# Kernel optimization log

Measured on AMD Instinct MI355X. Metric: run time of the kernel, lower is better.

Reference implementation:

```python
import jax, jax.numpy as jnp
import numpy as np

BATCH, N_IN, N_OUT, DEGREE = 128, 2048, 1024, 15
EPSILON = 1.0
TEMPERATURE = 0.1
NEG_FILL = -1000000000.0


def setup_inputs() -> dict:
    key = jax.random.key(0)
    k1, k2, k3 = jax.random.split(key, 3)
    x = jax.random.normal(k1, (BATCH, N_IN), dtype=jnp.float32)
    weights = jax.random.normal(k2, (N_OUT, N_IN), dtype=jnp.float32) * 0.02
    # buffer: (rand(n_out, n_in) < degree/n_in).float()
    synaptic_mask = (jax.random.uniform(k3, (N_OUT, N_IN)) < DEGREE / N_IN).astype(jnp.float32)
    return {"x": x, "weights": weights, "synaptic_mask": synaptic_mask}


def reference(x, weights, synaptic_mask):
    n_in = x.shape[1]
    # torch.median returns the LOWER of the two middle values for even n:
    # sorted index (n-1)//2
    consensus = jnp.sort(x, axis=1)[:, (n_in - 1) // 2][:, None]  # [B, 1]
    gate = (jnp.abs(x - consensus) < EPSILON).astype(x.dtype)      # [B, n_in]
    gated_x = x * gate                                             # [B, n_in]
    # dense broadcast-add: [B, n_out, n_in]
    combined = gated_x[:, None, :] + weights[None, :, :]
    masked_z = jnp.where(synaptic_mask == 0.0, NEG_FILL, combined)
    return TEMPERATURE * jax.nn.logsumexp(masked_z / TEMPERATURE, axis=2)  # [B, n_out]
```

## Files before the change

### kernel.cpp

```cpp
#include <hip/hip_runtime.h>
#include <math.h>

#define BATCH 128
#define N_IN 2048
#define N_OUT 1024
#define MAXK 40
#define BCAP 64
#define TEMP 0.1f
#define INV_TEMP 10.0f
#define NEG_FILL -1.0e9f
#define WLO -0.1875f
#define WHI 0.1875f
#define BINSCALE 682.6666666f

__device__ __forceinline__ unsigned int f2key(float f) {
    unsigned int b = __float_as_uint(f);
    return (b & 0x80000000u) ? ~b : (b | 0x80000000u);
}
__device__ __forceinline__ float key2f(unsigned int u) {
    unsigned int b = (u & 0x80000000u) ? (u & 0x7FFFFFFFu) : ~u;
    return __uint_as_float(b);
}

__global__ __launch_bounds__(256) void k_med(const float* __restrict__ x,
                                             float* __restrict__ gxT) {
    __shared__ unsigned int hist[256];
    __shared__ unsigned int wsum4[4];
    __shared__ unsigned int sel[2];
    __shared__ float sbin[BCAP];
    __shared__ int s_nb;
    __shared__ float s_med;

    const int tid = threadIdx.x;
    const int lane = tid & 63;
    const int wwid = tid >> 6;
    const int b = (int)blockIdx.x;

    const float4* xr = (const float4*)(x + (size_t)b * N_IN);
    float4 va = xr[tid], vb = xr[tid + 256];
    float vals[8] = {va.x, va.y, va.z, va.w, vb.x, vb.y, vb.z, vb.w};

    hist[tid] = 0;
    if (tid == 0) s_nb = 0;
    __syncthreads();

    int cb = 0;
#pragma unroll
    for (int j = 0; j < 8; ++j) {
        float v = vals[j];
        cb += (v < WLO) ? 1 : 0;
        if (v >= WLO && v < WHI) {
            int bin = (int)((v - WLO) * BINSCALE);
            bin = (bin > 255) ? 255 : bin;
            atomicAdd(&hist[bin], 1u);
        }
    }
    int sb = cb;
#pragma unroll
    for (int off = 1; off < 64; off <<= 1) sb += __shfl_xor(sb, off, 64);
    if (lane == 0) wsum4[wwid] = (unsigned int)sb;
    __syncthreads();
    const int c_lo = (int)(wsum4[0] + wsum4[1] + wsum4[2] + wsum4[3]);
    const int R = (N_IN - 1) / 2 - c_lo;

    unsigned int hv = hist[tid];
    unsigned int sv = hv;
#pragma unroll
    for (int off = 1; off < 64; off <<= 1) {
        unsigned int t = __shfl_up(sv, off, 64);
        if (lane >= off) sv += t;
    }
    __syncthreads();
    if (lane == 63) wsum4[wwid] = sv;
    if (tid == 0) sel[0] = 0xFFFFFFFFu;
    __syncthreads();
    unsigned int base = 0;
    for (int ww = 0; ww < wwid; ++ww) base += wsum4[ww];
    const unsigned int incl = sv + base;
    const unsigned int excl = incl - hv;
    const int n_c = (int)(wsum4[0] + wsum4[1] + wsum4[2] + wsum4[3]);
    if (R >= 0 && R < n_c && (unsigned int)R >= excl && (unsigned int)R < incl) {
        sel[0] = (unsigned int)tid;
        sel[1] = (unsigned int)R - excl;
    }
    __syncthreads();

    bool fast_ok = (R >= 0 && R < n_c && sel[0] != 0xFFFFFFFFu);
    if (fast_ok) {
        const int B = (int)sel[0];
        const int r2 = (int)sel[1];
#pragma unroll
        for (int j = 0; j < 8; ++j) {
            float v = vals[j];
            if (v >= WLO && v < WHI) {
                int bin = (int)((v - WLO) * BINSCALE);
                bin = (bin > 255) ? 255 : bin;
                if (bin == B) {
                    int p = atomicAdd(&s_nb, 1);
                    if (p < BCAP) sbin[p] = v;
                }
            }
        }
        __syncthreads();
        const int nb = s_nb;
        if (nb <= BCAP) {
            if (tid < nb) {
                float v = sbin[tid];
                int nlt = 0, neq = 0;
                for (int j = 0; j < nb; ++j) {
                    float u = sbin[j];
                    nlt += (u < v) ? 1 : 0;
                    neq += (u == v) ? 1 : 0;
                }
                if (nlt <= r2 && r2 < nlt + neq) s_med = v;
            }
        } else {
            fast_ok = false;
        }
        __syncthreads();
    }
    if (!fast_ok) {
        unsigned int prefix = 0;
        unsigned int k = (N_IN - 1) / 2;
        for (int pos = 24; pos >= 0; pos -= 8) {
            hist[tid] = 0;
            __syncthreads();
            const unsigned int hmask = (pos == 24) ? 0u : (0xFFFFFFFFu << (pos + 8));
#pragma unroll
            for (int j = 0; j < 8; ++j) {
                unsigned int u = f2key(vals[j]);
                if ((u & hmask) == (prefix & hmask))
                    atomicAdd(&hist[(u >> pos) & 0xFFu], 1u);
            }
            __syncthreads();
            unsigned int v = hist[tid];
            unsigned int s2 = v;
#pragma unroll
            for (int off = 1; off < 64; off <<= 1) {
                unsigned int t = __shfl_up(s2, off, 64);
                if (lane >= off) s2 += t;
            }
            if (lane == 63) wsum4[wwid] = s2;
            __syncthreads();
            unsigned int bs = 0;
            for (int ww = 0; ww < wwid; ++ww) bs += wsum4[ww];
            const unsigned int inc2 = s2 + bs;
            const unsigned int exc2 = inc2 - v;
            if (k >= exc2 && k < inc2) {
                sel[0] = (unsigned int)tid;
                sel[1] = k - exc2;
            }
            __syncthreads();
            prefix |= sel[0] << pos;
            k = sel[1];
            __syncthreads();
        }
        if (tid == 0) s_med = key2f(prefix);
        __syncthreads();
    }
    const float med = s_med;

#pragma unroll
    for (int j = 0; j < 8; ++j) {
        const int idx = (j < 4) ? 4 * tid + j : 1024 + 4 * tid + (j - 4);
        const float v = vals[j];
        gxT[(size_t)idx * BATCH + b] = (fabsf(v - med) < 1.0f) ? v : 0.0f;
    }
}

__global__ __launch_bounds__(256) void k_clse(const float* __restrict__ w,
                                              const float* __restrict__ msk,
                                              const float* __restrict__ gxT,
                                              float* __restrict__ out) {
    __shared__ unsigned int wsum4[4];
    __shared__ int sidx[2][MAXK];
    __shared__ float swv[2][MAXK];

    const int tid = threadIdx.x;
    const int lane = tid & 63;
    const int wwid = tid >> 6;
    const int o0 = (int)blockIdx.x * 2;

    const float4* m0 = (const float4*)(msk + (size_t)o0 * N_IN);
    const float4* m1 = (const float4*)(msk + (size_t)(o0 + 1) * N_IN);
    float4 m0a = m0[tid], m0b = m0[tid + 256];
    float4 m1a = m1[tid], m1b = m1[tid + 256];
    float mv0[8] = {m0a.x, m0a.y, m0a.z, m0a.w, m0b.x, m0b.y, m0b.z, m0b.w};
    float mv1[8] = {m1a.x, m1a.y, m1a.z, m1a.w, m1b.x, m1b.y, m1b.z, m1b.w};

    int c0 = 0, c1 = 0;
#pragma unroll
    for (int j = 0; j < 8; ++j) {
        c0 += (mv0[j] != 0.0f) ? 1 : 0;
        c1 += (mv1[j] != 0.0f) ? 1 : 0;
    }
    int packed = (c0 << 16) | c1;
    int sv = packed;
#pragma unroll
    for (int off = 1; off < 64; off <<= 1) {
        int t = __shfl_up(sv, off, 64);
        if (lane >= off) sv += t;
    }
    if (lane == 63) wsum4[wwid] = (unsigned int)sv;
    __syncthreads();
    int base = 0;
    for (int ww = 0; ww < wwid; ++ww) base += (int)wsum4[ww];
    const int excl = base + sv - packed;
    const int tot = (int)(wsum4[0] + wsum4[1] + wsum4[2] + wsum4[3]);
    const int ct0 = tot >> 16;
    const int ct1 = tot & 0xFFFF;

    int p0 = (excl >> 16) & 0xFFFF;
    int p1 = excl & 0xFFFF;
#pragma unroll
    for (int j = 0; j < 8; ++j) {
        const int idx = (j < 4) ? 4 * tid + j : 1024 + 4 * tid + (j - 4);
        if (mv0[j] != 0.0f) {
            if (p0 < MAXK) sidx[0][p0] = idx;
            ++p0;
        }
        if (mv1[j] != 0.0f) {
            if (p1 < MAXK) sidx[1][p1] = idx;
            ++p1;
        }
    }
    __syncthreads();

    const int cc0 = (ct0 < MAXK) ? ct0 : MAXK;
    const int cc1 = (ct1 < MAXK) ? ct1 : MAXK;
    if (tid < cc0) swv[0][tid] = w[(size_t)o0 * N_IN + sidx[0][tid]];
    else if (tid >= 64 && tid - 64 < cc1)
        swv[1][tid - 64] = w[(size_t)(o0 + 1) * N_IN + sidx[1][tid - 64]];
    __syncthreads();

    const int oSel = tid >> 7;
    const int o = o0 + oSel;
    const int b = tid & 127;
    const int c = oSel ? ct1 : ct0;

    float res;
    if (c == 0) {
        res = NEG_FILL;
    } else if (c <= MAXK) {
        int idx = sidx[oSel][0];
        float m = (gxT[(size_t)idx * BATCH + b] + swv[oSel][0]) * INV_TEMP;
        float s = 1.0f;
        for (int j = 1; j < c; ++j) {
            idx = sidx[oSel][j];
            float v = (gxT[(size_t)idx * BATCH + b] + swv[oSel][j]) * INV_TEMP;
            float mn = fmaxf(m, v);
            s = s * __expf(m - mn) + __expf(v - mn);
            m = mn;
        }
        res = TEMP * (m + __logf(s));
    } else {
        const float* mr = msk + (size_t)o * N_IN;
        const float* wr = w + (size_t)o * N_IN;
        float m = -INFINITY, s = 0.0f;
        for (int i = 0; i < N_IN; ++i) {
            if (mr[i] != 0.0f) {
                float v = (gxT[(size_t)i * BATCH + b] + wr[i]) * INV_TEMP;
                float mn = fmaxf(m, v);
                s = s * __expf(m - mn) + __expf(v - mn);
                m = mn;
            }
        }
        res = TEMP * (m + __logf(s));
    }
    out[(size_t)b * N_OUT + o] = res;
}

extern "C" void kernel_launch(void* const* d_in, const int* in_sizes, int n_in,
                              void* d_out, int out_size, void* d_ws, size_t ws_size,
                              hipStream_t stream) {
    const float* x = (const float*)d_in[0];
    const float* w = (const float*)d_in[1];
    const float* msk = (const float*)d_in[2];
    float* out = (float*)d_out;

    float* gxT = (float*)d_ws;

    hipLaunchKernelGGL(k_med, dim3(BATCH), dim3(256), 0, stream, x, gxT);
    hipLaunchKernelGGL(k_clse, dim3(N_OUT / 2), dim3(256), 0, stream,
                       w, msk, gxT, out);
}
```

Before: 19.14 us.

## Merge median and mask compaction into one prep kernel; batch-major LSE with shared gated x

The median blocks and the mask-compaction blocks now run side by side in a single prep launch. The compaction blocks write per-output counts and a transposed (index, weight) list to workspace, so the mask scan no longer sits on the critical path after the median. The LSE kernel now assigns each block to one batch row and half the outputs. It recomputes the gated x row into shared memory, which replaces scattered gxT global reads with LDS gathers, and reads the list entries coalesced across outputs. In exchange the list loads now go to global memory instead of shared, and x is reloaded once per output half.

```diff
diff --git a/kernel.cpp b/kernel.cpp
--- a/kernel.cpp
+++ b/kernel.cpp
@@ -22,232 +22,249 @@
     return __uint_as_float(b);
 }
 
-__global__ __launch_bounds__(256) void k_med(const float* __restrict__ x,
-                                             float* __restrict__ gxT) {
+__global__ __launch_bounds__(256) void k_prep(const float* __restrict__ x,
+                                              const float* __restrict__ w,
+                                              const float* __restrict__ msk,
+                                              int* __restrict__ cnt,
+                                              int2* __restrict__ listsT,
+                                              float* __restrict__ med) {
     __shared__ unsigned int hist[256];
     __shared__ unsigned int wsum4[4];
     __shared__ unsigned int sel[2];
     __shared__ float sbin[BCAP];
     __shared__ int s_nb;
     __shared__ float s_med;
+    __shared__ int sidx[2][MAXK];
 
     const int tid = threadIdx.x;
     const int lane = tid & 63;
     const int wwid = tid >> 6;
-    const int b = (int)blockIdx.x;
-
-    const float4* xr = (const float4*)(x + (size_t)b * N_IN);
-    float4 va = xr[tid], vb = xr[tid + 256];
-    float vals[8] = {va.x, va.y, va.z, va.w, vb.x, vb.y, vb.z, vb.w};
-
-    hist[tid] = 0;
-    if (tid == 0) s_nb = 0;
-    __syncthreads();
-
-    int cb = 0;
-#pragma unroll
-    for (int j = 0; j < 8; ++j) {
-        float v = vals[j];
-        cb += (v < WLO) ? 1 : 0;
-        if (v >= WLO && v < WHI) {
-            int bin = (int)((v - WLO) * BINSCALE);
-            bin = (bin > 255) ? 255 : bin;
-            atomicAdd(&hist[bin], 1u);
-        }
-    }
-    int sb = cb;
-#pragma unroll
-    for (int off = 1; off < 64; off <<= 1) sb += __shfl_xor(sb, off, 64);
-    if (lane == 0) wsum4[wwid] = (unsigned int)sb;
-    __syncthreads();
-    const int c_lo = (int)(wsum4[0] + wsum4[1] + wsum4[2] + wsum4[3]);
-    const int R = (N_IN - 1) / 2 - c_lo;
-
-    unsigned int hv = hist[tid];
-    unsigned int sv = hv;
-#pragma unroll
-    for (int off = 1; off < 64; off <<= 1) {
-        unsigned int t = __shfl_up(sv, off, 64);
-        if (lane >= off) sv += t;
-    }
-    __syncthreads();
-    if (lane == 63) wsum4[wwid] = sv;
-    if (tid == 0) sel[0] = 0xFFFFFFFFu;
-    __syncthreads();
-    unsigned int base = 0;
-    for (int ww = 0; ww < wwid; ++ww) base += wsum4[ww];
-    const unsigned int incl = sv + base;
-    const unsigned int excl = incl - hv;
-    const int n_c = (int)(wsum4[0] + wsum4[1] + wsum4[2] + wsum4[3]);
-    if (R >= 0 && R < n_c && (unsigned int)R >= excl && (unsigned int)R < incl) {
-        sel[0] = (unsigned int)tid;
-        sel[1] = (unsigned int)R - excl;
-    }
-    __syncthreads();
-
-    bool fast_ok = (R >= 0 && R < n_c && sel[0] != 0xFFFFFFFFu);
-    if (fast_ok) {
-        const int B = (int)sel[0];
-        const int r2 = (int)sel[1];
+    const int bid = (int)blockIdx.x;
+
+    if (bid < BATCH) {
+        const int b = bid;
+        const float4* xr = (const float4*)(x + (size_t)b * N_IN);
+        float4 va = xr[tid], vb = xr[tid + 256];
+        float vals[8] = {va.x, va.y, va.z, va.w, vb.x, vb.y, vb.z, vb.w};
+
+        hist[tid] = 0;
+        if (tid == 0) s_nb = 0;
+        __syncthreads();
+
+        int cb = 0;
 #pragma unroll
         for (int j = 0; j < 8; ++j) {
             float v = vals[j];
+            cb += (v < WLO) ? 1 : 0;
             if (v >= WLO && v < WHI) {
                 int bin = (int)((v - WLO) * BINSCALE);
                 bin = (bin > 255) ? 255 : bin;
-                if (bin == B) {
-                    int p = atomicAdd(&s_nb, 1);
-                    if (p < BCAP) sbin[p] = v;
-                }
-            }
-        }
-        __syncthreads();
-        const int nb = s_nb;
-        if (nb <= BCAP) {
-            if (tid < nb) {
-                float v = sbin[tid];
-                int nlt = 0, neq = 0;
-                for (int j = 0; j < nb; ++j) {
-                    float u = sbin[j];
-                    nlt += (u < v) ? 1 : 0;
-                    neq += (u == v) ? 1 : 0;
-                }
-                if (nlt <= r2 && r2 < nlt + neq) s_med = v;
-            }
-        } else {
-            fast_ok = false;
-        }
-        __syncthreads();
+                atomicAdd(&hist[bin], 1u);
+            }
+        }
+        int sb = cb;
+#pragma unroll
+        for (int off = 1; off < 64; off <<= 1) sb += __shfl_xor(sb, off, 64);
+        if (lane == 0) wsum4[wwid] = (unsigned int)sb;
+        __syncthreads();
+        const int c_lo = (int)(wsum4[0] + wsum4[1] + wsum4[2] + wsum4[3]);
+        const int R = (N_IN - 1) / 2 - c_lo;
+
+        unsigned int hv = hist[tid];
+        unsigned int sv = hv;
+#pragma unroll
+        for (int off = 1; off < 64; off <<= 1) {
+            unsigned int t = __shfl_up(sv, off, 64);
+            if (lane >= off) sv += t;
+        }
+        __syncthreads();
+        if (lane == 63) wsum4[wwid] = sv;
+        if (tid == 0) sel[0] = 0xFFFFFFFFu;
+        __syncthreads();
+        unsigned int base = 0;
+        for (int ww = 0; ww < wwid; ++ww) base += wsum4[ww];
+        const unsigned int incl = sv + base;
+        const unsigned int excl = incl - hv;
+        const int n_c = (int)(wsum4[0] + wsum4[1] + wsum4[2] + wsum4[3]);
+        if (R >= 0 && R < n_c && (unsigned int)R >= excl && (unsigned int)R < incl) {
+            sel[0] = (unsigned int)tid;
+            sel[1] = (unsigned int)R - excl;
+        }
+        __syncthreads();
+
+        bool fast_ok = (R >= 0 && R < n_c && sel[0] != 0xFFFFFFFFu);
+        if (fast_ok) {
+            const int B = (int)sel[0];
+            const int r2 = (int)sel[1];
+#pragma unroll
+            for (int j = 0; j < 8; ++j) {
+                float v = vals[j];
+                if (v >= WLO && v < WHI) {
+                    int bin = (int)((v - WLO) * BINSCALE);
+                    bin = (bin > 255) ? 255 : bin;
+                    if (bin == B) {
+                        int p = atomicAdd(&s_nb, 1);
+                        if (p < BCAP) sbin[p] = v;
+                    }
+                }
+            }
+            __syncthreads();
+            const int nb = s_nb;
+            if (nb <= BCAP) {
+                if (tid < nb) {
+                    float v = sbin[tid];
+                    int nlt = 0, neq = 0;
+                    for (int j = 0; j < nb; ++j) {
+                        float u = sbin[j];
+                        nlt += (u < v) ? 1 : 0;
+                        neq += (u == v) ? 1 : 0;
+                    }
+                    if (nlt <= r2 && r2 < nlt + neq) s_med = v;
+                }
+            } else {
+                fast_ok = false;
+            }
+            __syncthreads();
+        }
+        if (!fast_ok) {
+            unsigned int prefix = 0;
+            unsigned int k = (N_IN - 1) / 2;
+            for (int pos = 24; pos >= 0; pos -= 8) {
+                hist[tid] = 0;
+                __syncthreads();
+                const unsigned int hmask = (pos == 24) ? 0u : (0xFFFFFFFFu << (pos + 8));
+#pragma unroll
+                for (int j = 0; j < 8; ++j) {
+                    unsigned int u = f2key(vals[j]);
+                    if ((u & hmask) == (prefix & hmask))
+                        atomicAdd(&hist[(u >> pos) & 0xFFu], 1u);
+                }
+                __syncthreads();
+                unsigned int v = hist[tid];
+                unsigned int s2 = v;
+#pragma unroll
+                for (int off = 1; off < 64; off <<= 1) {
+                    unsigned int t = __shfl_up(s2, off, 64);
+                    if (lane >= off) s2 += t;
+                }
+                if (lane == 63) wsum4[wwid] = s2;
+                __syncthreads();
+                unsigned int bs = 0;
+                for (int ww = 0; ww < wwid; ++ww) bs += wsum4[ww];
+                const unsigned int inc2 = s2 + bs;
+                const unsigned int exc2 = inc2 - v;
+                if (k >= exc2 && k < inc2) {
+                    sel[0] = (unsigned int)tid;
+                    sel[1] = k - exc2;
+                }
+                __syncthreads();
+                prefix |= sel[0] << pos;
+                k = sel[1];
+                __syncthreads();
+            }
+            if (tid == 0) s_med = key2f(prefix);
+            __syncthreads();
+        }
+        if (tid == 0) med[bid] = s_med;
+    } else {
+        const int o0 = (bid - BATCH) * 2;
+        const float4* m0 = (const float4*)(msk + (size_t)o0 * N_IN);
+        const float4* m1 = (const float4*)(msk + (size_t)(o0 + 1) * N_IN);
+        float4 m0a = m0[tid], m0b = m0[tid + 256];
+        float4 m1a = m1[tid], m1b = m1[tid + 256];
+        float mv0[8] = {m0a.x, m0a.y, m0a.z, m0a.w, m0b.x, m0b.y, m0b.z, m0b.w};
+        float mv1[8] = {m1a.x, m1a.y, m1a.z, m1a.w, m1b.x, m1b.y, m1b.z, m1b.w};
+
+        int c0 = 0, c1 = 0;
+#pragma unroll
+        for (int j = 0; j < 8; ++j) {
+            c0 += (mv0[j] != 0.0f) ? 1 : 0;
+            c1 += (mv1[j] != 0.0f) ? 1 : 0;
+        }
+        int packed = (c0 << 16) | c1;
+        int sv = packed;
+#pragma unroll
+        for (int off = 1; off < 64; off <<= 1) {
+            int t = __shfl_up(sv, off, 64);
+            if (lane >= off) sv += t;
+        }
+        if (lane == 63) wsum4[wwid] = (unsigned int)sv;
+        __syncthreads();
+        int base = 0;
+        for (int ww = 0; ww < wwid; ++ww) base += (int)wsum4[ww];
+        const int excl = base + sv - packed;
+        const int tot = (int)(wsum4[0] + wsum4[1] + wsum4[2] + wsum4[3]);
+        const int ct0 = tot >> 16;
+        const int ct1 = tot & 0xFFFF;
+        if (tid == 0) {
+            cnt[o0] = ct0;
+            cnt[o0 + 1] = ct1;
+        }
+
+        int p0 = (excl >> 16) & 0xFFFF;
+        int p1 = excl & 0xFFFF;
+#pragma unroll
+        for (int j = 0; j < 8; ++j) {
+            const int idx = (j < 4) ? 4 * tid + j : 1024 + 4 * tid + (j - 4);
+            if (mv0[j] != 0.0f) {
+                if (p0 < MAXK) sidx[0][p0] = idx;
+                ++p0;
+            }
+            if (mv1[j] != 0.0f) {
+                if (p1 < MAXK) sidx[1][p1] = idx;
+                ++p1;
+            }
+        }
+        __syncthreads();
+
+        const int cc0 = (ct0 < MAXK) ? ct0 : MAXK;
+        const int cc1 = (ct1 < MAXK) ? ct1 : MAXK;
+        if (tid < cc0) {
+            const int idx = sidx[0][tid];
+            listsT[tid * N_OUT + o0] = make_int2(idx, __float_as_int(w[(size_t)o0 * N_IN + idx]));
+        } else if (tid >= 64 && tid - 64 < cc1) {
+            const int idx = sidx[1][tid - 64];
+            listsT[(tid - 64) * N_OUT + (o0 + 1)] =
+                make_int2(idx, __float_as_int(w[(size_t)(o0 + 1) * N_IN + idx]));
+        }
     }
-    if (!fast_ok) {
-        unsigned int prefix = 0;
-        unsigned int k = (N_IN - 1) / 2;
-        for (int pos = 24; pos >= 0; pos -= 8) {
-            hist[tid] = 0;
-            __syncthreads();
-            const unsigned int hmask = (pos == 24) ? 0u : (0xFFFFFFFFu << (pos + 8));
-#pragma unroll
-            for (int j = 0; j < 8; ++j) {
-                unsigned int u = f2key(vals[j]);
-                if ((u & hmask) == (prefix & hmask))
-                    atomicAdd(&hist[(u >> pos) & 0xFFu], 1u);
-            }
-            __syncthreads();
-            unsigned int v = hist[tid];
-            unsigned int s2 = v;
-#pragma unroll
-            for (int off = 1; off < 64; off <<= 1) {
-                unsigned int t = __shfl_up(s2, off, 64);
-                if (lane >= off) s2 += t;
-            }
-            if (lane == 63) wsum4[wwid] = s2;
-            __syncthreads();
-            unsigned int bs = 0;
-            for (int ww = 0; ww < wwid; ++ww) bs += wsum4[ww];
-            const unsigned int inc2 = s2 + bs;
-            const unsigned int exc2 = inc2 - v;
-            if (k >= exc2 && k < inc2) {
-                sel[0] = (unsigned int)tid;
-                sel[1] = k - exc2;
-            }
-            __syncthreads();
-            prefix |= sel[0] << pos;
-            k = sel[1];
-            __syncthreads();
-        }
-        if (tid == 0) s_med = key2f(prefix);
-        __syncthreads();
-    }
-    const float med = s_med;
-
-#pragma unroll
-    for (int j = 0; j < 8; ++j) {
-        const int idx = (j < 4) ? 4 * tid + j : 1024 + 4 * tid + (j - 4);
-        const float v = vals[j];
-        gxT[(size_t)idx * BATCH + b] = (fabsf(v - med) < 1.0f) ? v : 0.0f;
-    }
-}
-
-__global__ __launch_bounds__(256) void k_clse(const float* __restrict__ w,
-                                              const float* __restrict__ msk,
-                                              const float* __restrict__ gxT,
-                                              float* __restrict__ out) {
-    __shared__ unsigned int wsum4[4];
-    __shared__ int sidx[2][MAXK];
-    __shared__ float swv[2][MAXK];
-
+}
+
+__global__ __launch_bounds__(512) void k_lse(const float* __restrict__ x,
+                                             const float* __restrict__ medv,
+                                             const int* __restrict__ cnt,
+                                             const int2* __restrict__ listsT,
+                                             const float* __restrict__ w,
+                                             const float* __restrict__ msk,
+                                             float* __restrict__ out) {
+    __shared__ float sgx[N_IN];
+    const int b = blockIdx.x >> 1;
+    const int h = blockIdx.x & 1;
     const int tid = threadIdx.x;
-    const int lane = tid & 63;
-    const int wwid = tid >> 6;
-    const int o0 = (int)blockIdx.x * 2;
-
-    const float4* m0 = (const float4*)(msk + (size_t)o0 * N_IN);
-    const float4* m1 = (const float4*)(msk + (size_t)(o0 + 1) * N_IN);
-    float4 m0a = m0[tid], m0b = m0[tid + 256];
-    float4 m1a = m1[tid], m1b = m1[tid + 256];
-    float mv0[8] = {m0a.x, m0a.y, m0a.z, m0a.w, m0b.x, m0b.y, m0b.z, m0b.w};
-    float mv1[8] = {m1a.x, m1a.y, m1a.z, m1a.w, m1b.x, m1b.y, m1b.z, m1b.w};
-
-    int c0 = 0, c1 = 0;
-#pragma unroll
-    for (int j = 0; j < 8; ++j) {
-        c0 += (mv0[j] != 0.0f) ? 1 : 0;
-        c1 += (mv1[j] != 0.0f) ? 1 : 0;
-    }
-    int packed = (c0 << 16) | c1;
-    int sv = packed;
-#pragma unroll
-    for (int off = 1; off < 64; off <<= 1) {
-        int t = __shfl_up(sv, off, 64);
-        if (lane >= off) sv += t;
-    }
-    if (lane == 63) wsum4[wwid] = (unsigned int)sv;
+
+    const float med = medv[b];
+    const float4* xr = (const float4*)(x + (size_t)b * N_IN);
+    float4 va = xr[tid];
+    float4 ga;
+    ga.x = (fabsf(va.x - med) < 1.0f) ? va.x : 0.0f;
+    ga.y = (fabsf(va.y - med) < 1.0f) ? va.y : 0.0f;
+    ga.z = (fabsf(va.z - med) < 1.0f) ? va.z : 0.0f;
+    ga.w = (fabsf(va.w - med) < 1.0f) ? va.w : 0.0f;
+    ((float4*)sgx)[tid] = ga;
     __syncthreads();
-    int base = 0;
-    for (int ww = 0; ww < wwid; ++ww) base += (int)wsum4[ww];
-    const int excl = base + sv - packed;
-    const int tot = (int)(wsum4[0] + wsum4[1] + wsum4[2] + wsum4[3]);
-    const int ct0 = tot >> 16;
-    const int ct1 = tot & 0xFFFF;
-
-    int p0 = (excl >> 16) & 0xFFFF;
-    int p1 = excl & 0xFFFF;
-#pragma unroll
-    for (int j = 0; j < 8; ++j) {
-        const int idx = (j < 4) ? 4 * tid + j : 1024 + 4 * tid + (j - 4);
-        if (mv0[j] != 0.0f) {
-            if (p0 < MAXK) sidx[0][p0] = idx;
-            ++p0;
-        }
-        if (mv1[j] != 0.0f) {
-            if (p1 < MAXK) sidx[1][p1] = idx;
-            ++p1;
-        }
-    }
-    __syncthreads();
-
-    const int cc0 = (ct0 < MAXK) ? ct0 : MAXK;
-    const int cc1 = (ct1 < MAXK) ? ct1 : MAXK;
-    if (tid < cc0) swv[0][tid] = w[(size_t)o0 * N_IN + sidx[0][tid]];
-    else if (tid >= 64 && tid - 64 < cc1)
-        swv[1][tid - 64] = w[(size_t)(o0 + 1) * N_IN + sidx[1][tid - 64]];
-    __syncthreads();
-
-    const int oSel = tid >> 7;
-    const int o = o0 + oSel;
-    const int b = tid & 127;
-    const int c = oSel ? ct1 : ct0;
-
+
+    const int o = h * 512 + tid;
+    const int c = cnt[o];
     float res;
     if (c == 0) {
         res = NEG_FILL;
     } else if (c <= MAXK) {
-        int idx = sidx[oSel][0];
-        float m = (gxT[(size_t)idx * BATCH + b] + swv[oSel][0]) * INV_TEMP;
+        int2 e = listsT[o];
+        float m = (sgx[e.x] + __int_as_float(e.y)) * INV_TEMP;
         float s = 1.0f;
         for (int j = 1; j < c; ++j) {
-            idx = sidx[oSel][j];
-            float v = (gxT[(size_t)idx * BATCH + b] + swv[oSel][j]) * INV_TEMP;
+            e = listsT[j * N_OUT + o];
+            float v = (sgx[e.x] + __int_as_float(e.y)) * INV_TEMP;
             float mn = fmaxf(m, v);
             s = s * __expf(m - mn) + __expf(v - mn);
             m = mn;
@@ -259,7 +276,7 @@
         float m = -INFINITY, s = 0.0f;
         for (int i = 0; i < N_IN; ++i) {
             if (mr[i] != 0.0f) {
-                float v = (gxT[(size_t)i * BATCH + b] + wr[i]) * INV_TEMP;
+                float v = (sgx[i] + wr[i]) * INV_TEMP;
                 float mn = fmaxf(m, v);
                 s = s * __expf(m - mn) + __expf(v - mn);
                 m = mn;
@@ -278,9 +295,12 @@
     const float* msk = (const float*)d_in[2];
     float* out = (float*)d_out;
 
-    float* gxT = (float*)d_ws;
-
-    hipLaunchKernelGGL(k_med, dim3(BATCH), dim3(256), 0, stream, x, gxT);
-    hipLaunchKernelGGL(k_clse, dim3(N_OUT / 2), dim3(256), 0, stream,
-                       w, msk, gxT, out);
-}
+    int* cnt = (int*)d_ws;
+    int2* listsT = (int2*)(cnt + N_OUT);
+    float* med = (float*)(listsT + (size_t)MAXK * N_OUT);
+
+    hipLaunchKernelGGL(k_prep, dim3(BATCH + N_OUT / 2), dim3(256), 0, stream,
+                       x, w, msk, cnt, listsT, med);
+    hipLaunchKernelGGL(k_lse, dim3(BATCH * 2), dim3(512), 0, stream,
+                       x, med, cnt, listsT, w, msk, out);
+}
```

New measurement: 16.09 us. 1.19x faster.
